# Kernel optimization log

Measured on AMD Instinct MI355X. Metric: run time of the kernel, lower is better.

Reference implementation:

```python
import jax, jax.numpy as jnp
import numpy as np
import math

B, N, HID, NH = 128, 512, 512, 8
DH = HID // NH  # d_heads = 64


def setup_inputs() -> dict:
    key = jax.random.key(0)
    ks = jax.random.split(key, 8)
    s = 0.05  # keep logits in a sane range
    h = jax.random.normal(ks[0], (B, N, HID), dtype=jnp.float32)
    lengths = jax.random.randint(ks[1], (B,), 1, N + 1, dtype=jnp.int32)
    w_q = jax.random.normal(ks[2], (HID, HID), dtype=jnp.float32) * s
    w_k = jax.random.normal(ks[3], (HID, HID), dtype=jnp.float32) * s
    w_v = jax.random.normal(ks[4], (HID, HID), dtype=jnp.float32) * s
    w_o = jax.random.normal(ks[5], (HID, HID), dtype=jnp.float32) * s
    w_seed_w = jax.random.normal(ks[6], (HID, 1), dtype=jnp.float32) * s  # Linear(1, k*hidden), k=1
    w_seed_b = jax.random.normal(ks[7], (HID,), dtype=jnp.float32) * s
    seed_vec = jnp.ones((1,), dtype=jnp.float32)
    return {"h": h, "lengths": lengths, "w_q": w_q, "w_k": w_k, "w_v": w_v,
            "w_o": w_o, "w_seed_w": w_seed_w, "w_seed_b": w_seed_b, "seed_vec": seed_vec}


def reference(h, lengths, w_q, w_k, w_v, w_o, w_seed_w, w_seed_b, seed_vec):
    # PMA with k=1 seed query. norm_features=False.
    # query = w_seed(seed_vec), same for every graph in the batch.
    query = w_seed_w @ seed_vec + w_seed_b            # [HID]
    q = (w_q @ query).reshape(NH, DH)                 # [NH, DH] (Linear: x @ W.T == W @ x for vector)
    # NOTE: original code computes w_k(v) but never uses it in attention; output
    # depends only on q and v (e = q * v summed over d_heads). We skip the dead compute.
    v = (h @ w_v.T).reshape(B, N, NH, DH)             # [B, N, NH, DH]
    # logits: e[b,h,n] = <q[h], v[b,n,h]> / sqrt(DH)
    e = jnp.einsum("hd,bnhd->bhn", q, v) / math.sqrt(DH)
    valid = jnp.arange(N)[None, :] < lengths[:, None]  # [B, N] ragged mask
    e = jnp.where(valid[:, None, :], e, -jnp.inf)
    alpha = jax.nn.softmax(e, axis=-1)                # [B, NH, N]; padded cols -> 0
    out_h = jnp.einsum("bhn,bnhd->bhd", alpha, v)     # [B, NH, DH]
    out = out_h.reshape(B, HID) @ w_o.T               # [B*k, HID], packed (k=1)
    alpha_out = alpha[..., None]                      # [B, NH, N, 1] matching torch permute
    return out, alpha_out
```

## Files before the change

kernel.cpp:

```cpp
#include <hip/hip_runtime.h>
#include <math.h>

constexpr int B = 128, N = 512, HID = 512, NH = 8, DH = 64;

__global__ __launch_bounds__(64) void k1_qk(
    const float* __restrict__ w_q, const float* __restrict__ w_v,
    const float* __restrict__ w_sw, const float* __restrict__ w_sb,
    const float* __restrict__ seed, float* __restrict__ qk)
{
    __shared__ __align__(16) float query_s[HID];
    __shared__ float q_s[DH];
    const int t  = threadIdx.x;
    const int h  = blockIdx.x >> 3;
    const int jc = blockIdx.x & 7;
    const float sv = seed[0];
    #pragma unroll
    for (int k = 0; k < 8; ++k) {
        const int j = t * 8 + k;
        query_s[j] = w_sw[j] * sv + w_sb[j];
    }
    __syncthreads();
    {
        const float* row = w_q + (size_t)(h * DH + t) * HID;
        float acc = 0.f;
        for (int j = 0; j < HID; j += 4) {
            const float4 wv = *(const float4*)(row + j);
            acc += wv.x * query_s[j]     + wv.y * query_s[j + 1]
                 + wv.z * query_s[j + 2] + wv.w * query_s[j + 3];
        }
        q_s[t] = acc;
    }
    __syncthreads();
    {
        const int j = jc * 64 + t;
        float acc = 0.f;
        for (int d = 0; d < DH; ++d)
            acc += q_s[d] * w_v[(size_t)(h * DH + d) * HID + j];
        qk[h * HID + j] = acc * 0.125f;
    }
}

__global__ __launch_bounds__(256) void ke_logits(
    const float* __restrict__ hbuf, const int* __restrict__ lengths,
    const float* __restrict__ qk, float* __restrict__ e_ws)
{
    const int t    = threadIdx.x;
    const int b    = blockIdx.x >> 1;
    const int half = blockIdx.x & 1;
    const int len  = lengths[b];
    const int n    = half * 256 + t;
    const int n0   = half * 256 + (t & ~63);
    if (n0 >= len) return;

    const int nn = min(n, len - 1);
    const float* row = hbuf + ((size_t)b * N + nn) * HID;
    float acc[NH];
    #pragma unroll
    for (int hh = 0; hh < NH; ++hh) acc[hh] = 0.f;

    #pragma unroll 8
    for (int j = 0; j < HID; j += 4) {
        const float4 hv = *(const float4*)(row + j);
        #pragma unroll
        for (int hh = 0; hh < NH; ++hh) {
            const float* qp = qk + hh * HID + j;
            acc[hh] += hv.x * qp[0] + hv.y * qp[1]
                     + hv.z * qp[2] + hv.w * qp[3];
        }
    }
    if (n < len) {
        #pragma unroll
        for (int hh = 0; hh < NH; ++hh)
            e_ws[(size_t)(b * NH + hh) * N + n] = acc[hh];
    }
}

__global__ __launch_bounds__(256) void ks_softmax(
    const float* __restrict__ e_ws, const int* __restrict__ lengths,
    float* __restrict__ alpha, float* __restrict__ al_t)
{
    const int b    = blockIdx.x;
    const int lane = threadIdx.x & 63;
    const int w    = threadIdx.x >> 6;
    const int len  = lengths[b];
    for (int hh = w; hh < NH; hh += 4) {
        const float* e = e_ws + (size_t)(b * NH + hh) * N;
        float ev[8];
        float m = -3.0e38f;
        #pragma unroll
        for (int it = 0; it < 8; ++it) {
            const int n = it * 64 + lane;
            ev[it] = (n < len) ? e[n] : -3.0e38f;
            m = fmaxf(m, ev[it]);
        }
        #pragma unroll
        for (int off = 32; off; off >>= 1)
            m = fmaxf(m, __shfl_xor(m, off, 64));
        float s = 0.f;
        #pragma unroll
        for (int it = 0; it < 8; ++it) {
            ev[it] = __expf(ev[it] - m);
            s += ev[it];
        }
        #pragma unroll
        for (int off = 32; off; off >>= 1)
            s += __shfl_xor(s, off, 64);
        const float inv = 1.f / s;
        float* ao = alpha + (size_t)(b * NH + hh) * N;
        float* at = al_t + (size_t)b * N * NH + hh;
        #pragma unroll
        for (int it = 0; it < 8; ++it) {
            const int n   = it * 64 + lane;
            const float v = (n < len) ? ev[it] * inv : 0.f;
            ao[n]      = v;
            at[n * NH] = v;
        }
    }
}

__global__ __launch_bounds__(256) void kc_ctx(
    const float* __restrict__ hbuf, const int* __restrict__ lengths,
    const float* __restrict__ al_t, float* __restrict__ ctxp)
{
    const int t   = threadIdx.x;
    const int b   = blockIdx.x >> 3;
    const int c   = blockIdx.x & 7;
    const int n0  = c * 64;
    const int g   = t >> 7;
    const int cq  = t & 127;
    const int len = lengths[b];
    const int nend = min(len - n0, 64);

    float4 acc[NH];
    #pragma unroll
    for (int hh = 0; hh < NH; ++hh) { acc[hh].x = acc[hh].y = acc[hh].z = acc[hh].w = 0.f; }

    const float* hb = hbuf + ((size_t)b * N + n0) * HID + cq * 4;
    const float* ap = al_t + ((size_t)b * N + n0) * NH;
    #pragma unroll 4
    for (int ln = g; ln < nend; ln += 2) {
        const float4 hv = *(const float4*)(hb + (size_t)ln * HID);
        const float* a = ap + ln * NH;
        acc[0].x += a[0] * hv.x; acc[0].y += a[0] * hv.y; acc[0].z += a[0] * hv.z; acc[0].w += a[0] * hv.w;
        acc[1].x += a[1] * hv.x; acc[1].y += a[1] * hv.y; acc[1].z += a[1] * hv.z; acc[1].w += a[1] * hv.w;
        acc[2].x += a[2] * hv.x; acc[2].y += a[2] * hv.y; acc[2].z += a[2] * hv.z; acc[2].w += a[2] * hv.w;
        acc[3].x += a[3] * hv.x; acc[3].y += a[3] * hv.y; acc[3].z += a[3] * hv.z; acc[3].w += a[3] * hv.w;
        acc[4].x += a[4] * hv.x; acc[4].y += a[4] * hv.y; acc[4].z += a[4] * hv.z; acc[4].w += a[4] * hv.w;
        acc[5].x += a[5] * hv.x; acc[5].y += a[5] * hv.y; acc[5].z += a[5] * hv.z; acc[5].w += a[5] * hv.w;
        acc[6].x += a[6] * hv.x; acc[6].y += a[6] * hv.y; acc[6].z += a[6] * hv.z; acc[6].w += a[6] * hv.w;
        acc[7].x += a[7] * hv.x; acc[7].y += a[7] * hv.y; acc[7].z += a[7] * hv.z; acc[7].w += a[7] * hv.w;
    }
    float* cp = ctxp + (size_t)(((b * 8 + c) * 2 + g) * NH) * HID + cq * 4;
    #pragma unroll
    for (int hh = 0; hh < NH; ++hh)
        *(float4*)(cp + (size_t)hh * HID) = acc[hh];
}

__global__ __launch_bounds__(256) void kd_out(
    const float* __restrict__ ctxp, const float* __restrict__ w_v,
    const float* __restrict__ w_o, float* __restrict__ out)
{
    __shared__ __align__(16) float ctx_s[NH * HID];
    __shared__ __align__(16) float oh_s[HID];
    const int t = threadIdx.x;
    const int b = blockIdx.x;
    const float* p0 = ctxp + (size_t)(b * 16) * NH * HID;
    for (int i = t; i < NH * HID; i += 256) {
        float s = 0.f;
        #pragma unroll
        for (int cc = 0; cc < 16; ++cc) s += p0[(size_t)cc * NH * HID + i];
        ctx_s[i] = s;
    }
    __syncthreads();
    #pragma unroll
    for (int rep = 0; rep < 2; ++rep) {
        const int p  = rep * 256 + t;
        const int hh = p >> 6;
        const float* wrow = w_v + (size_t)p * HID;
        float acc = 0.f;
        for (int j = 0; j < HID; j += 4) {
            const float4 wv = *(const float4*)(wrow + j);
            const float4 cv = *(const float4*)&ctx_s[hh * HID + j];
            acc += wv.x * cv.x + wv.y * cv.y + wv.z * cv.z + wv.w * cv.w;
        }
        oh_s[p] = acc;
    }
    __syncthreads();
    #pragma unroll
    for (int rep = 0; rep < 2; ++rep) {
        const int i = rep * 256 + t;
        const float* wrow = w_o + (size_t)i * HID;
        float acc = 0.f;
        for (int j = 0; j < HID; j += 4) {
            const float4 wv = *(const float4*)(wrow + j);
            const float4 ov = *(const float4*)&oh_s[j];
            acc += wv.x * ov.x + wv.y * ov.y + wv.z * ov.z + wv.w * ov.w;
        }
        out[(size_t)b * HID + i] = acc;
    }
}

extern "C" void kernel_launch(void* const* d_in, const int* in_sizes, int n_in,
                              void* d_out, int out_size, void* d_ws, size_t ws_size,
                              hipStream_t stream) {
    const float* h     = (const float*)d_in[0];
    const int*   lens  = (const int*)  d_in[1];
    const float* w_q   = (const float*)d_in[2];
    const float* w_v   = (const float*)d_in[4];
    const float* w_o   = (const float*)d_in[5];
    const float* w_sw  = (const float*)d_in[6];
    const float* w_sb  = (const float*)d_in[7];
    const float* seed  = (const float*)d_in[8];

    float* out   = (float*)d_out;
    float* alpha = out + (size_t)B * HID;

    float* ws   = (float*)d_ws;
    float* qk   = ws;
    float* e_ws = qk + NH * HID;
    float* al_t = e_ws + (size_t)B * NH * N;
    float* ctxp = al_t + (size_t)B * N * NH;

    hipLaunchKernelGGL(k1_qk,      dim3(64),    dim3(64),  0, stream,
                       w_q, w_v, w_sw, w_sb, seed, qk);
    hipLaunchKernelGGL(ke_logits,  dim3(B * 2), dim3(256), 0, stream,
                       h, lens, qk, e_ws);
    hipLaunchKernelGGL(ks_softmax, dim3(B),     dim3(256), 0, stream,
                       e_ws, lens, alpha, al_t);
    hipLaunchKernelGGL(kc_ctx,     dim3(B * 8), dim3(256), 0, stream,
                       h, lens, al_t, ctxp);
    hipLaunchKernelGGL(kd_out,     dim3(B),     dim3(256), 0, stream,
                       ctxp, w_v, w_o, out);
}
```

Measured before the change: 331.6 us.

## Restructure logits kernel to wave-per-row with coalesced loads and shuffle reduction

The logits kernel now gives each wavefront a whole row of h. Each lane loads two coalesced float4 slices and holds its slice of all 8 qk vectors in registers. Per-head partial dots are combined with a transposing butterfly shuffle reduction. Previously each thread streamed its own 2KB row, so a wave's loads were strided across rows and the qk operand was re-read every iteration. The grid grows to 8 blocks per batch, and the softmax kernel is split across 2 blocks per batch to raise parallelism, at the cost of more shuffle work per row.

```diff
diff --git a/kernel.cpp b/kernel.cpp
--- a/kernel.cpp
+++ b/kernel.cpp
@@ -44,34 +44,61 @@
     const float* __restrict__ hbuf, const int* __restrict__ lengths,
     const float* __restrict__ qk, float* __restrict__ e_ws)
 {
-    const int t    = threadIdx.x;
-    const int b    = blockIdx.x >> 1;
-    const int half = blockIdx.x & 1;
-    const int len  = lengths[b];
-    const int n    = half * 256 + t;
-    const int n0   = half * 256 + (t & ~63);
+    const int t = threadIdx.x;
+    const int l = t & 63;
+    const int w = t >> 6;
+    const int b = blockIdx.x >> 3;
+    const int c = blockIdx.x & 7;
+    const int n0 = c * 64;
+    const int len = lengths[b];
     if (n0 >= len) return;
 
-    const int nn = min(n, len - 1);
-    const float* row = hbuf + ((size_t)b * N + nn) * HID;
-    float acc[NH];
-    #pragma unroll
-    for (int hh = 0; hh < NH; ++hh) acc[hh] = 0.f;
-
-    #pragma unroll 8
-    for (int j = 0; j < HID; j += 4) {
-        const float4 hv = *(const float4*)(row + j);
-        #pragma unroll
-        for (int hh = 0; hh < NH; ++hh) {
-            const float* qp = qk + hh * HID + j;
-            acc[hh] += hv.x * qp[0] + hv.y * qp[1]
-                     + hv.z * qp[2] + hv.w * qp[3];
-        }
-    }
-    if (n < len) {
+    float4 qlo[NH], qhi[NH];
+    #pragma unroll
+    for (int hh = 0; hh < NH; ++hh) {
+        qlo[hh] = *(const float4*)&qk[hh * HID + l * 4];
+        qhi[hh] = *(const float4*)&qk[hh * HID + 256 + l * 4];
+    }
+
+    const int nmax = min(n0 + 64, len);
+    const float* hb = hbuf + (size_t)b * N * HID;
+    const int hh_out = ((l & 1) << 2) | (l & 2) | ((l >> 2) & 1);
+
+    for (int n = n0 + w; n < nmax; n += 4) {
+        const float* row = hb + (size_t)n * HID;
+        const float4 h0 = *(const float4*)(row + l * 4);
+        const float4 h1 = *(const float4*)(row + 256 + l * 4);
+        float v[NH];
         #pragma unroll
         for (int hh = 0; hh < NH; ++hh)
-            e_ws[(size_t)(b * NH + hh) * N + n] = acc[hh];
+            v[hh] = h0.x * qlo[hh].x + h0.y * qlo[hh].y
+                  + h0.z * qlo[hh].z + h0.w * qlo[hh].w
+                  + h1.x * qhi[hh].x + h1.y * qhi[hh].y
+                  + h1.z * qhi[hh].z + h1.w * qhi[hh].w;
+
+        #pragma unroll
+        for (int i = 0; i < 4; ++i) {
+            const float ax = __shfl_xor(v[i], 1, 64);
+            const float bx = __shfl_xor(v[i + 4], 1, 64);
+            v[i] = (l & 1) ? (v[i + 4] + bx) : (v[i] + ax);
+        }
+        #pragma unroll
+        for (int i = 0; i < 2; ++i) {
+            const float ax = __shfl_xor(v[i], 2, 64);
+            const float bx = __shfl_xor(v[i + 2], 2, 64);
+            v[i] = (l & 2) ? (v[i + 2] + bx) : (v[i] + ax);
+        }
+        {
+            const float ax = __shfl_xor(v[0], 4, 64);
+            const float bx = __shfl_xor(v[1], 4, 64);
+            v[0] = (l & 4) ? (v[1] + bx) : (v[0] + ax);
+        }
+        v[0] += __shfl_xor(v[0], 8, 64);
+        v[0] += __shfl_xor(v[0], 16, 64);
+        v[0] += __shfl_xor(v[0], 32, 64);
+
+        if (l < 8)
+            e_ws[(size_t)(b * NH + hh_out) * N + n] = v[0];
     }
 }
 
@@ -79,42 +106,42 @@
     const float* __restrict__ e_ws, const int* __restrict__ lengths,
     float* __restrict__ alpha, float* __restrict__ al_t)
 {
-    const int b    = blockIdx.x;
+    const int b    = blockIdx.x >> 1;
+    const int grp  = blockIdx.x & 1;
     const int lane = threadIdx.x & 63;
-    const int w    = threadIdx.x >> 6;
+    const int hh   = grp * 4 + (threadIdx.x >> 6);
     const int len  = lengths[b];
-    for (int hh = w; hh < NH; hh += 4) {
-        const float* e = e_ws + (size_t)(b * NH + hh) * N;
-        float ev[8];
-        float m = -3.0e38f;
-        #pragma unroll
-        for (int it = 0; it < 8; ++it) {
-            const int n = it * 64 + lane;
-            ev[it] = (n < len) ? e[n] : -3.0e38f;
-            m = fmaxf(m, ev[it]);
-        }
-        #pragma unroll
-        for (int off = 32; off; off >>= 1)
-            m = fmaxf(m, __shfl_xor(m, off, 64));
-        float s = 0.f;
-        #pragma unroll
-        for (int it = 0; it < 8; ++it) {
-            ev[it] = __expf(ev[it] - m);
-            s += ev[it];
-        }
-        #pragma unroll
-        for (int off = 32; off; off >>= 1)
-            s += __shfl_xor(s, off, 64);
-        const float inv = 1.f / s;
-        float* ao = alpha + (size_t)(b * NH + hh) * N;
-        float* at = al_t + (size_t)b * N * NH + hh;
-        #pragma unroll
-        for (int it = 0; it < 8; ++it) {
-            const int n   = it * 64 + lane;
-            const float v = (n < len) ? ev[it] * inv : 0.f;
-            ao[n]      = v;
-            at[n * NH] = v;
-        }
+
+    const float* e = e_ws + (size_t)(b * NH + hh) * N;
+    float ev[8];
+    float m = -3.0e38f;
+    #pragma unroll
+    for (int it = 0; it < 8; ++it) {
+        const int n = it * 64 + lane;
+        ev[it] = (n < len) ? e[n] : -3.0e38f;
+        m = fmaxf(m, ev[it]);
+    }
+    #pragma unroll
+    for (int off = 32; off; off >>= 1)
+        m = fmaxf(m, __shfl_xor(m, off, 64));
+    float s = 0.f;
+    #pragma unroll
+    for (int it = 0; it < 8; ++it) {
+        ev[it] = __expf(ev[it] - m);
+        s += ev[it];
+    }
+    #pragma unroll
+    for (int off = 32; off; off >>= 1)
+        s += __shfl_xor(s, off, 64);
+    const float inv = 1.f / s;
+    float* ao = alpha + (size_t)(b * NH + hh) * N;
+    float* at = al_t + (size_t)b * N * NH + hh;
+    #pragma unroll
+    for (int it = 0; it < 8; ++it) {
+        const int n   = it * 64 + lane;
+        const float v = (n < len) ? ev[it] * inv : 0.f;
+        ao[n]      = v;
+        at[n * NH] = v;
     }
 }
 
@@ -223,9 +250,9 @@
 
     hipLaunchKernelGGL(k1_qk,      dim3(64),    dim3(64),  0, stream,
                        w_q, w_v, w_sw, w_sb, seed, qk);
-    hipLaunchKernelGGL(ke_logits,  dim3(B * 2), dim3(256), 0, stream,
+    hipLaunchKernelGGL(ke_logits,  dim3(B * 8), dim3(256), 0, stream,
                        h, lens, qk, e_ws);
-    hipLaunchKernelGGL(ks_softmax, dim3(B),     dim3(256), 0, stream,
+    hipLaunchKernelGGL(ks_softmax, dim3(B * 2), dim3(256), 0, stream,
                        e_ws, lens, alpha, al_t);
     hipLaunchKernelGGL(kc_ctx,     dim3(B * 8), dim3(256), 0, stream,
                        h, lens, al_t, ctxp);
```

Measured after the change: 305.1 us. 1.09x faster.
